# Performance work log

Measured on AMD Instinct MI355X. Metric: run time of the kernel, lower is better.

The kernel has to match this reference:

```python
import jax, jax.numpy as jnp
import numpy as np

N_NODES = 100000
N_EDGES = 3200000
F_IN = 128
F_HID = 32
F_OUT = 40


def gcn_conv(x, edge_index, edge_weight, W, b):
    # GCNConv with normalize=False: linear transform, then edge-weighted
    # gather from source nodes and scatter-add into destination nodes.
    h = x @ W                                   # [N, F_out]
    src, dst = edge_index[0], edge_index[1]
    msgs = h[src] * edge_weight[:, None]        # [E, F_out] gather + scale
    agg = jax.ops.segment_sum(msgs, dst, num_segments=N_NODES)
    return agg + b


def setup_inputs() -> dict:
    key = jax.random.key(0)
    k1, k2, k3, k4, k5, k6, k7 = jax.random.split(key, 7)
    x = jax.random.normal(k1, (N_NODES, F_IN), dtype=jnp.float32)
    edge_index = jax.random.randint(k2, (2, N_EDGES), 0, N_NODES, dtype=jnp.int64)
    edge_weight = jax.random.uniform(k3, (N_EDGES,), dtype=jnp.float32)
    # Glorot-style init for layer weights, zeros for biases (PyG defaults)
    W1 = jax.random.normal(k4, (F_IN, F_HID), dtype=jnp.float32) * (1.0 / np.sqrt(F_IN))
    b1 = jnp.zeros((F_HID,), dtype=jnp.float32)
    W2 = jax.random.normal(k5, (F_HID, F_OUT), dtype=jnp.float32) * (1.0 / np.sqrt(F_HID))
    b2 = jnp.zeros((F_OUT,), dtype=jnp.float32)
    return {"x": x, "edge_index": edge_index, "edge_weight": edge_weight,
            "W1": W1, "b1": b1, "W2": W2, "b2": b2}


def reference(x, edge_index, edge_weight, W1, b1, W2, b2):
    h = gcn_conv(x, edge_index, edge_weight, W1, b1)
    h = jax.nn.relu(h)
    # F.dropout(training=self.training) is identity in eval mode
    h = gcn_conv(h, edge_index, edge_weight, W2, b2)
    return jax.nn.log_softmax(h, axis=1)
```

## Files before the change

kernel.cpp:

```cpp
#include <hip/hip_runtime.h>
#include <hip/hip_fp16.h>
#include <math.h>

#define N_NODES 100000
#define N_EDGES 3200000
#define F_IN    128
#define F_HID   32
#define F_OUT   40
#define NBINS   ((N_NODES + 255) >> 8)
#define EPB     4096
#define NBLK    ((N_EDGES + EPB - 1) / EPB)
#define SRC_SPLIT 50000
#define CAPH    (N_EDGES / 2 + 8 * N_NODES)

typedef _Float16 h2_t __attribute__((ext_vector_type(2)));
__device__ __forceinline__ float fdot2u(unsigned a, unsigned b, float c) {
    return __builtin_amdgcn_fdot2(__builtin_bit_cast(h2_t, a),
                                  __builtin_bit_cast(h2_t, b), c, false);
}

__global__ __launch_bounds__(256) void gemm1_kernel(const float* __restrict__ x,
                                                    const float* __restrict__ W,
                                                    __half* __restrict__ h1h) {
    __shared__ float Ws[F_IN * F_HID];
    __shared__ float Xs[32][F_IN + 4];
    const int tid  = threadIdx.x;
    const int row0 = blockIdx.x * 32;

    for (int i = tid; i < (F_IN * F_HID) / 4; i += 256)
        ((float4*)Ws)[i] = ((const float4*)W)[i];

    for (int i = tid; i < 1024; i += 256) {
        int r = i >> 5;
        int c = i & 31;
        ((float4*)&Xs[r][0])[c] = ((const float4*)x)[(size_t)(row0 + r) * (F_IN / 4) + c];
    }
    __syncthreads();

    const int r  = tid >> 3;
    const int c0 = (tid & 7) * 4;
    float a0 = 0.f, a1 = 0.f, a2 = 0.f, a3 = 0.f;
    for (int k = 0; k < F_IN; ++k) {
        const float xv = Xs[r][k];
        const float* wrow = &Ws[k * F_HID + c0];
        a0 += xv * wrow[0];
        a1 += xv * wrow[1];
        a2 += xv * wrow[2];
        a3 += xv * wrow[3];
    }
    const int row = row0 + r;
    __half2* o = (__half2*)(h1h + (size_t)row * F_HID + c0);
    o[0] = __floats2half2_rn(a0, a1);
    o[1] = __floats2half2_rn(a2, a3);
}

__global__ __launch_bounds__(256) void histA_kernel(const int* __restrict__ ei,
                                                    int* __restrict__ gcnt) {
    __shared__ int lh[NBINS];
    const int tid = threadIdx.x;
    const int e0  = blockIdx.x * EPB;
    for (int i = tid; i < NBINS; i += 256) lh[i] = 0;
    __syncthreads();

    for (int base = 0; base < EPB; base += 1024) {
        const int e = e0 + base + 4 * tid;
        if (e + 3 < N_EDGES) {
            const int4 dv = *(const int4*)&ei[N_EDGES + e];
            atomicAdd(&lh[dv.x >> 8], 1);
            atomicAdd(&lh[dv.y >> 8], 1);
            atomicAdd(&lh[dv.z >> 8], 1);
            atomicAdd(&lh[dv.w >> 8], 1);
        } else {
            for (int k = 0; k < 4; ++k)
                if (e + k < N_EDGES) atomicAdd(&lh[ei[N_EDGES + e + k] >> 8], 1);
        }
    }
    __syncthreads();
    for (int b = tid; b < NBINS; b += 256)
        gcnt[(size_t)blockIdx.x * NBINS + b] = lh[b];
}

__global__ __launch_bounds__(256) void colscan_kernel(const int* __restrict__ gcnt,
                                                      int* __restrict__ pbase,
                                                      int* __restrict__ bintot) {
    __shared__ int s[256];
    __shared__ int carry;
    const int b   = blockIdx.x;
    const int tid = threadIdx.x;
    if (tid == 0) carry = 0;
    __syncthreads();
    for (int c = 0; c < NBLK; c += 256) {
        const int blk = c + tid;
        const int v = (blk < NBLK) ? gcnt[(size_t)blk * NBINS + b] : 0;
        s[tid] = v;
        __syncthreads();
        for (int off = 1; off < 256; off <<= 1) {
            int u = (tid >= off) ? s[tid - off] : 0;
            __syncthreads();
            s[tid] += u;
            __syncthreads();
        }
        if (blk < NBLK) pbase[(size_t)blk * NBINS + b] = carry + s[tid] - v;
        __syncthreads();
        if (tid == 255) carry += s[255];
        __syncthreads();
    }
    if (tid == 0) bintot[b] = carry;
}

__global__ __launch_bounds__(512) void binscan_kernel(const int* __restrict__ bintot,
                                                      int* __restrict__ binbase) {
    __shared__ int s[512];
    const int t = threadIdx.x;
    const int v = (t < NBINS) ? bintot[t] : 0;
    s[t] = v;
    __syncthreads();
    for (int off = 1; off < 512; off <<= 1) {
        int u = (t >= off) ? s[t - off] : 0;
        __syncthreads();
        s[t] += u;
        __syncthreads();
    }
    if (t <= NBINS) binbase[t] = s[t] - v;
}

__global__ __launch_bounds__(256) void placeA_kernel(const int* __restrict__ ei,
                                                     const float* __restrict__ ew,
                                                     const int* __restrict__ gcnt,
                                                     const int* __restrict__ binbase,
                                                     const int* __restrict__ pbase,
                                                     int* __restrict__ stg4,
                                                     unsigned short* __restrict__ metag) {
    __shared__ int lhist[512];
    __shared__ int lscan[512];
    __shared__ int lcur[512];
    __shared__ int lwbase[512];
    __shared__ int stmp[256];
    __shared__ int lstg4[EPB];
    __shared__ unsigned short lbin[EPB];
    __shared__ unsigned short lmeta[EPB];
    const int tid = threadIdx.x;
    const int blk = blockIdx.x;
    const int e0  = blk * EPB;
    const int tot = min(EPB, N_EDGES - e0);

    lhist[tid] = 0; lhist[tid + 256] = 0;
    lwbase[tid] = 0; lwbase[tid + 256] = 0;
    __syncthreads();
    for (int b = tid; b < NBINS; b += 256) {
        lhist[b]  = gcnt[(size_t)blk * NBINS + b];
        lwbase[b] = binbase[b] + pbase[(size_t)blk * NBINS + b];
    }
    __syncthreads();

    const int ca = lhist[2 * tid];
    const int cb = lhist[2 * tid + 1];
    const int pair = ca + cb;
    stmp[tid] = pair;
    __syncthreads();
    for (int off = 1; off < 256; off <<= 1) {
        int u = (tid >= off) ? stmp[tid - off] : 0;
        __syncthreads();
        stmp[tid] += u;
        __syncthreads();
    }
    const int pexcl = stmp[tid] - pair;
    lscan[2 * tid]     = pexcl;
    lscan[2 * tid + 1] = pexcl + ca;
    lcur[2 * tid]      = pexcl;
    lcur[2 * tid + 1]  = pexcl + ca;
    __syncthreads();

#define PLACE1(S, D, WF)                                                        \
    {                                                                           \
        const int b = (D) >> 8;                                                 \
        const int p = atomicAdd(&lcur[b], 1);                                   \
        lstg4[p] = (S) | ((int)__half_as_ushort(__float2half(WF)) << 17);       \
        lbin[p] = (unsigned short)b;                                            \
        lmeta[p] = (unsigned short)(((D) & 255) | (((S) >= SRC_SPLIT) << 8));   \
    }
    for (int base = 0; base < EPB; base += 1024) {
        const int e = e0 + base + 4 * tid;
        if (e + 3 < N_EDGES) {
            const int4   sv = *(const int4*)&ei[e];
            const int4   dv = *(const int4*)&ei[N_EDGES + e];
            const float4 wv = *(const float4*)&ew[e];
            PLACE1(sv.x, dv.x, wv.x);
            PLACE1(sv.y, dv.y, wv.y);
            PLACE1(sv.z, dv.z, wv.z);
            PLACE1(sv.w, dv.w, wv.w);
        } else {
            for (int k = 0; k < 4; ++k)
                if (e + k < N_EDGES)
                    PLACE1(ei[e + k], ei[N_EDGES + e + k], ew[e + k]);
        }
    }
#undef PLACE1
    __syncthreads();

    for (int i = tid; i < tot; i += 256) {
        const int b = lbin[i];
        const int pos = lwbase[b] + (i - lscan[b]);
        stg4[pos] = lstg4[i];
        metag[pos] = lmeta[i];
    }
}

__global__ __launch_bounds__(256) void partB1_kernel(const int* __restrict__ binbase,
                                                     const unsigned short* __restrict__ metag,
                                                     int* __restrict__ offsIBA,
                                                     int* __restrict__ offsIBB,
                                                     int* __restrict__ pbtA,
                                                     int* __restrict__ pbtB) {
    __shared__ int lcA[256], lcB[256], lsc[256];
    const int tid   = threadIdx.x;
    const int b     = blockIdx.x;
    const int start = binbase[b];
    const int end   = binbase[b + 1];

    lcA[tid] = 0; lcB[tid] = 0;
    __syncthreads();
    for (int j = start + tid; j < end; j += 256) {
        const unsigned m = metag[j];
        if (m & 256) atomicAdd(&lcB[m & 255], 1);
        else         atomicAdd(&lcA[m & 255], 1);
    }
    __syncthreads();

    const int padA = (lcA[tid] + 7) & ~7;
    lsc[tid] = padA;
    __syncthreads();
    for (int off = 1; off < 256; off <<= 1) {
        int u = (tid >= off) ? lsc[tid - off] : 0;
        __syncthreads();
        lsc[tid] += u;
        __syncthreads();
    }
    offsIBA[(b << 8) + tid] = lsc[tid] - padA;
    if (tid == 255) pbtA[b] = lsc[255];
    __syncthreads();

    const int padB = (lcB[tid] + 7) & ~7;
    lsc[tid] = padB;
    __syncthreads();
    for (int off = 1; off < 256; off <<= 1) {
        int u = (tid >= off) ? lsc[tid - off] : 0;
        __syncthreads();
        lsc[tid] += u;
        __syncthreads();
    }
    offsIBB[(b << 8) + tid] = lsc[tid] - padB;
    if (tid == 255) pbtB[b] = lsc[255];
}

__global__ __launch_bounds__(512) void padscan2_kernel(const int* __restrict__ pbtA,
                                                       const int* __restrict__ pbtB,
                                                       int* __restrict__ pbbA,
                                                       int* __restrict__ pbbB,
                                                       int* __restrict__ offsA,
                                                       int* __restrict__ offsB) {
    __shared__ int s[512];
    const int t = threadIdx.x;
    {
        const int v = (t < NBINS) ? pbtA[t] : 0;
        s[t] = v;
        __syncthreads();
        for (int off = 1; off < 512; off <<= 1) {
            int u = (t >= off) ? s[t - off] : 0;
            __syncthreads();
            s[t] += u;
            __syncthreads();
        }
        if (t <= NBINS) pbbA[t] = s[t] - v;
        if (t == NBINS) offsA[N_NODES] = s[t] - v;
        __syncthreads();
    }
    {
        const int v = (t < NBINS) ? pbtB[t] : 0;
        s[t] = v;
        __syncthreads();
        for (int off = 1; off < 512; off <<= 1) {
            int u = (t >= off) ? s[t - off] : 0;
            __syncthreads();
            s[t] += u;
            __syncthreads();
        }
        if (t <= NBINS) pbbB[t] = s[t] - v;
        if (t == NBINS) offsB[N_NODES] = s[t] - v;
    }
}

__global__ __launch_bounds__(256) void partB2_kernel(const int* __restrict__ binbase,
                                                     const int* __restrict__ stg4,
                                                     const unsigned short* __restrict__ metag,
                                                     const int* __restrict__ pbbA,
                                                     const int* __restrict__ pbbB,
                                                     const int* __restrict__ offsIBA,
                                                     const int* __restrict__ offsIBB,
                                                     int* __restrict__ offsA,
                                                     int* __restrict__ offsB,
                                                     int* __restrict__ bktA,
                                                     int* __restrict__ bktB) {
    __shared__ int lcurA[256], lcurB[256];
    const int tid  = threadIdx.x;
    const int b    = blockIdx.x;
    const int node = (b << 8) + tid;
    const int baseA = pbbA[b] + offsIBA[node];
    const int baseB = pbbB[b] + offsIBB[node];
    const int pendA = (tid < 255) ? (pbbA[b] + offsIBA[node + 1]) : pbbA[b + 1];
    const int pendB = (tid < 255) ? (pbbB[b] + offsIBB[node + 1]) : pbbB[b + 1];
    lcurA[tid] = baseA;
    lcurB[tid] = baseB;
    if (node < N_NODES) { offsA[node] = baseA; offsB[node] = baseB; }
    __syncthreads();

    const int start = binbase[b];
    const int end   = binbase[b + 1];
    for (int j = start + tid; j < end; j += 256) {
        const int word = stg4[j];
        const unsigned m = metag[j];
        if (m & 256) {
            const int pos = atomicAdd(&lcurB[m & 255], 1);
            bktB[pos] = word;
        } else {
            const int pos = atomicAdd(&lcurA[m & 255], 1);
            bktA[pos] = word;
        }
    }
    __syncthreads();

    for (int k = lcurA[tid]; k < pendA; ++k) bktA[k] = 0;
    for (int k = lcurB[tid]; k < pendB; ++k) bktB[k] = SRC_SPLIT;
}

__device__ __forceinline__ void gather_grp(const int* __restrict__ bkt,
                                           int j, const int jend,
                                           const char* __restrict__ tbl,
                                           const unsigned sub8,
                                           float& a0, float& a1, float& a2, float& a3) {
#define PAIR_BODY(PX, PY, RA, RB)                                               \
    {                                                                           \
        const unsigned wp = __builtin_amdgcn_perm((unsigned)(PY) >> 17,         \
                                                  (unsigned)(PX) >> 17,         \
                                                  0x05040100u);                 \
        a0 = fdot2u(__builtin_amdgcn_perm((RB).x, (RA).x, 0x05040100u), wp, a0);\
        a1 = fdot2u(__builtin_amdgcn_perm((RB).x, (RA).x, 0x07060302u), wp, a1);\
        a2 = fdot2u(__builtin_amdgcn_perm((RB).y, (RA).y, 0x05040100u), wp, a2);\
        a3 = fdot2u(__builtin_amdgcn_perm((RB).y, (RA).y, 0x07060302u), wp, a3);\
    }
#define TBL(P) (*(const uint2*)(tbl + (((unsigned)(P) & 0x1FFFFu) << 6) + sub8))
    for (; j < jend; j += 8) {
        const int4 p0 = *(const int4*)&bkt[j];
        const int4 p1 = *(const int4*)&bkt[j + 4];
        const uint2 r0 = TBL(p0.x);
        const uint2 r1 = TBL(p0.y);
        const uint2 r2 = TBL(p0.z);
        const uint2 r3 = TBL(p0.w);
        const uint2 r4 = TBL(p1.x);
        const uint2 r5 = TBL(p1.y);
        const uint2 r6 = TBL(p1.z);
        const uint2 r7 = TBL(p1.w);
        PAIR_BODY(p0.x, p0.y, r0, r1);
        PAIR_BODY(p0.z, p0.w, r2, r3);
        PAIR_BODY(p1.x, p1.y, r4, r5);
        PAIR_BODY(p1.z, p1.w, r6, r7);
    }
#undef TBL
#undef PAIR_BODY
}

__global__ __launch_bounds__(256) void gather1_kernel(const int* __restrict__ offsA,
                                                      const int* __restrict__ offsB,
                                                      const int* __restrict__ bktA,
                                                      const int* __restrict__ bktB,
                                                      const __half* __restrict__ h1h,
                                                      const float* __restrict__ b1,
                                                      __half* __restrict__ rh) {
    const int tid  = threadIdx.x;
    const int node = blockIdx.x * 32 + (tid >> 3);
    const int sub  = tid & 7;
    const unsigned sub8 = sub * 8;

    float a0 = 0.f, a1 = 0.f, a2 = 0.f, a3 = 0.f;
    gather_grp(bktA, offsA[node], offsA[node + 1], (const char*)h1h, sub8,
               a0, a1, a2, a3);
    gather_grp(bktB, offsB[node], offsB[node + 1], (const char*)h1h, sub8,
               a0, a1, a2, a3);

    const float4 bb = ((const float4*)b1)[sub];
    a0 = fmaxf(a0 + bb.x, 0.f);
    a1 = fmaxf(a1 + bb.y, 0.f);
    a2 = fmaxf(a2 + bb.z, 0.f);
    a3 = fmaxf(a3 + bb.w, 0.f);
    uint2 o;
    *(__half2*)&o.x = __floats2half2_rn(a0, a1);
    *(__half2*)&o.y = __floats2half2_rn(a2, a3);
    *(uint2*)((char*)rh + (size_t)node * 64 + sub8) = o;
}

__global__ __launch_bounds__(256) void gather2_lsm_kernel(const int* __restrict__ offsA,
                                                          const int* __restrict__ offsB,
                                                          const int* __restrict__ bktA,
                                                          const int* __restrict__ bktB,
                                                          const __half* __restrict__ rh,
                                                          const float* __restrict__ W2,
                                                          const float* __restrict__ b2,
                                                          float* __restrict__ out) {
    __shared__ float W2s[F_HID * F_OUT];
    __shared__ float sblk[32][F_HID + 1];
    const int tid = threadIdx.x;
    for (int i = tid; i < F_HID * F_OUT; i += 256) W2s[i] = W2[i];
    __syncthreads();

    const int nn   = tid >> 3;
    const int node = blockIdx.x * 32 + nn;
    const int sub  = tid & 7;
    const unsigned sub8 = sub * 8;

    float a0 = 0.f, a1 = 0.f, a2 = 0.f, a3 = 0.f;
    gather_grp(bktA, offsA[node], offsA[node + 1], (const char*)rh, sub8,
               a0, a1, a2, a3);
    gather_grp(bktB, offsB[node], offsB[node + 1], (const char*)rh, sub8,
               a0, a1, a2, a3);

    sblk[nn][sub * 4 + 0] = a0;
    sblk[nn][sub * 4 + 1] = a1;
    sblk[nn][sub * 4 + 2] = a2;
    sblk[nn][sub * 4 + 3] = a3;

    float o0 = b2[sub], o1 = b2[sub + 8], o2 = b2[sub + 16],
          o3 = b2[sub + 24], o4 = b2[sub + 32];
    #pragma unroll
    for (int k = 0; k < F_HID; ++k) {
        const float sv = sblk[nn][k];
        const float* wr = &W2s[k * F_OUT + sub];
        o0 += sv * wr[0];
        o1 += sv * wr[8];
        o2 += sv * wr[16];
        o3 += sv * wr[24];
        o4 += sv * wr[32];
    }

    float m = fmaxf(fmaxf(fmaxf(o0, o1), fmaxf(o2, o3)), o4);
    m = fmaxf(m, __shfl_xor(m, 1));
    m = fmaxf(m, __shfl_xor(m, 2));
    m = fmaxf(m, __shfl_xor(m, 4));
    float ex = __expf(o0 - m) + __expf(o1 - m) + __expf(o2 - m)
             + __expf(o3 - m) + __expf(o4 - m);
    ex += __shfl_xor(ex, 1);
    ex += __shfl_xor(ex, 2);
    ex += __shfl_xor(ex, 4);
    const float ls = m + __logf(ex);

    float* op = out + (size_t)node * F_OUT + sub;
    op[0]  = o0 - ls;
    op[8]  = o1 - ls;
    op[16] = o2 - ls;
    op[24] = o3 - ls;
    op[32] = o4 - ls;
}

extern "C" void kernel_launch(void* const* d_in, const int* in_sizes, int n_in,
                              void* d_out, int out_size, void* d_ws, size_t ws_size,
                              hipStream_t stream) {
    const float* x  = (const float*)d_in[0];
    const int*   ei = (const int*)d_in[1];
    const float* ew = (const float*)d_in[2];
    const float* W1 = (const float*)d_in[3];
    const float* b1 = (const float*)d_in[4];
    const float* W2 = (const float*)d_in[5];
    const float* b2 = (const float*)d_in[6];
    float* out = (float*)d_out;

    char* p = (char*)d_ws;
    size_t off = 0;
    auto alloc = [&](size_t bytes) {
        char* r = p + off;
        off += (bytes + 15) & ~(size_t)15;
        return r;
    };
    int*   gcnt    = (int*)  alloc((size_t)NBLK * NBINS * 4);
    int*   pbase   = (int*)  alloc((size_t)NBLK * NBINS * 4);
    int*   bintot  = (int*)  alloc((size_t)NBINS * 4);
    int*   binbase = (int*)  alloc((size_t)(NBINS + 1) * 4);
    int*   pbtA    = (int*)  alloc((size_t)NBINS * 4);
    int*   pbtB    = (int*)  alloc((size_t)NBINS * 4);
    int*   pbbA    = (int*)  alloc((size_t)(NBINS + 1) * 4);
    int*   pbbB    = (int*)  alloc((size_t)(NBINS + 1) * 4);
    int*   offsIBA = (int*)  alloc((size_t)NBINS * 256 * 4);
    int*   offsIBB = (int*)  alloc((size_t)NBINS * 256 * 4);
    int*   offsA   = (int*)  alloc((size_t)(N_NODES + 1) * 4);
    int*   offsB   = (int*)  alloc((size_t)(N_NODES + 1) * 4);
    int*   bktA    = (int*)  alloc((size_t)CAPH * 4);
    int*   bktB    = (int*)  alloc((size_t)CAPH * 4);
    char*  uni     = (char*) alloc((size_t)N_EDGES * 6);
    int*   stg4    = (int*)uni;
    unsigned short* metag = (unsigned short*)(uni + (size_t)N_EDGES * 4);
    __half* h1h    = (__half*)uni;
    __half* rh     = h1h + (size_t)N_NODES * F_HID;

    histA_kernel<<<NBLK, 256, 0, stream>>>(ei, gcnt);
    colscan_kernel<<<NBINS, 256, 0, stream>>>(gcnt, pbase, bintot);
    binscan_kernel<<<1, 512, 0, stream>>>(bintot, binbase);
    placeA_kernel<<<NBLK, 256, 0, stream>>>(ei, ew, gcnt, binbase, pbase, stg4, metag);
    partB1_kernel<<<NBINS, 256, 0, stream>>>(binbase, metag, offsIBA, offsIBB, pbtA, pbtB);
    padscan2_kernel<<<1, 512, 0, stream>>>(pbtA, pbtB, pbbA, pbbB, offsA, offsB);
    partB2_kernel<<<NBINS, 256, 0, stream>>>(binbase, stg4, metag, pbbA, pbbB,
                                             offsIBA, offsIBB, offsA, offsB, bktA, bktB);

    gemm1_kernel<<<N_NODES / 32, 256, 0, stream>>>(x, W1, h1h);
    gather1_kernel<<<N_NODES / 32, 256, 0, stream>>>(offsA, offsB, bktA, bktB, h1h, b1, rh);

    gather2_lsm_kernel<<<N_NODES / 32, 256, 0, stream>>>(offsA, offsB, bktA, bktB, rh, W2, b2, out);
}
```

Before: 177.5 us.

## Sort nodes by padded degree class to balance gather work per block

Adds a counting sort of nodes by padded in-degree (histogram, scan, placement kernels) that produces a permutation. The two gather kernels then process nodes in permuted order, so nodes with similar edge counts share a wavefront and lanes diverge less in loop trip count. In exchange it launches three extra small kernels plus a memset, and the output writes per block become scattered rather than contiguous. With random uniform edges the degree spread is narrow, so there is little imbalance to remove.

```diff
diff --git a/kernel.cpp b/kernel.cpp
--- a/kernel.cpp
+++ b/kernel.cpp
@@ -12,6 +12,7 @@
 #define NBLK    ((N_EDGES + EPB - 1) / EPB)
 #define SRC_SPLIT 50000
 #define CAPH    (N_EDGES / 2 + 8 * N_NODES)
+#define NCLS    64
 
 typedef _Float16 h2_t __attribute__((ext_vector_type(2)));
 __device__ __forceinline__ float fdot2u(unsigned a, unsigned b, float c) {
@@ -333,6 +334,66 @@
     for (int k = lcurB[tid]; k < pendB; ++k) bktB[k] = SRC_SPLIT;
 }
 
+__global__ __launch_bounds__(256) void deghist_kernel(const int* __restrict__ offsA,
+                                                      const int* __restrict__ offsB,
+                                                      int* __restrict__ dcnt) {
+    __shared__ int lc[NCLS];
+    const int tid = threadIdx.x;
+    if (tid < NCLS) lc[tid] = 0;
+    __syncthreads();
+    const int n = blockIdx.x * 256 + tid;
+    if (n < N_NODES) {
+        const int len = (offsA[n + 1] - offsA[n]) + (offsB[n + 1] - offsB[n]);
+        atomicAdd(&lc[min(len >> 3, NCLS - 1)], 1);
+    }
+    __syncthreads();
+    if (tid < NCLS && lc[tid]) atomicAdd(&dcnt[tid], lc[tid]);
+}
+
+__global__ __launch_bounds__(64) void degscan_kernel(const int* __restrict__ dcnt,
+                                                     int* __restrict__ dcur) {
+    __shared__ int s[NCLS];
+    const int t = threadIdx.x;
+    const int v = dcnt[t];
+    s[t] = v;
+    __syncthreads();
+    for (int off = 1; off < NCLS; off <<= 1) {
+        int u = (t >= off) ? s[t - off] : 0;
+        __syncthreads();
+        s[t] += u;
+        __syncthreads();
+    }
+    dcur[t] = s[t] - v;
+}
+
+__global__ __launch_bounds__(256) void degplace_kernel(const int* __restrict__ offsA,
+                                                       const int* __restrict__ offsB,
+                                                       int* __restrict__ dcur,
+                                                       int* __restrict__ perm) {
+    __shared__ int lcnt[NCLS], lbase[NCLS];
+    const int tid = threadIdx.x;
+    if (tid < NCLS) lcnt[tid] = 0;
+    __syncthreads();
+    const int n = blockIdx.x * 256 + tid;
+    int cls = 0;
+    if (n < N_NODES) {
+        const int len = (offsA[n + 1] - offsA[n]) + (offsB[n + 1] - offsB[n]);
+        cls = min(len >> 3, NCLS - 1);
+        atomicAdd(&lcnt[cls], 1);
+    }
+    __syncthreads();
+    if (tid < NCLS) {
+        const int c = lcnt[tid];
+        lbase[tid] = c ? atomicAdd(&dcur[tid], c) : 0;
+        lcnt[tid] = 0;
+    }
+    __syncthreads();
+    if (n < N_NODES) {
+        const int r = atomicAdd(&lcnt[cls], 1);
+        perm[lbase[cls] + r] = n;
+    }
+}
+
 __device__ __forceinline__ void gather_grp(const int* __restrict__ bkt,
                                            int j, const int jend,
                                            const char* __restrict__ tbl,
@@ -369,7 +430,8 @@
 #undef PAIR_BODY
 }
 
-__global__ __launch_bounds__(256) void gather1_kernel(const int* __restrict__ offsA,
+__global__ __launch_bounds__(256) void gather1_kernel(const int* __restrict__ perm,
+                                                      const int* __restrict__ offsA,
                                                       const int* __restrict__ offsB,
                                                       const int* __restrict__ bktA,
                                                       const int* __restrict__ bktB,
@@ -377,7 +439,7 @@
                                                       const float* __restrict__ b1,
                                                       __half* __restrict__ rh) {
     const int tid  = threadIdx.x;
-    const int node = blockIdx.x * 32 + (tid >> 3);
+    const int node = perm[blockIdx.x * 32 + (tid >> 3)];
     const int sub  = tid & 7;
     const unsigned sub8 = sub * 8;
 
@@ -398,7 +460,8 @@
     *(uint2*)((char*)rh + (size_t)node * 64 + sub8) = o;
 }
 
-__global__ __launch_bounds__(256) void gather2_lsm_kernel(const int* __restrict__ offsA,
+__global__ __launch_bounds__(256) void gather2_lsm_kernel(const int* __restrict__ perm,
+                                                          const int* __restrict__ offsA,
                                                           const int* __restrict__ offsB,
                                                           const int* __restrict__ bktA,
                                                           const int* __restrict__ bktB,
@@ -413,7 +476,7 @@
     __syncthreads();
 
     const int nn   = tid >> 3;
-    const int node = blockIdx.x * 32 + nn;
+    const int node = perm[blockIdx.x * 32 + nn];
     const int sub  = tid & 7;
     const unsigned sub8 = sub * 8;
 
@@ -487,10 +550,13 @@
     int*   pbtB    = (int*)  alloc((size_t)NBINS * 4);
     int*   pbbA    = (int*)  alloc((size_t)(NBINS + 1) * 4);
     int*   pbbB    = (int*)  alloc((size_t)(NBINS + 1) * 4);
+    int*   dcnt    = (int*)  alloc((size_t)NCLS * 4);
+    int*   dcur    = (int*)  alloc((size_t)NCLS * 4);
     int*   offsIBA = (int*)  alloc((size_t)NBINS * 256 * 4);
     int*   offsIBB = (int*)  alloc((size_t)NBINS * 256 * 4);
     int*   offsA   = (int*)  alloc((size_t)(N_NODES + 1) * 4);
     int*   offsB   = (int*)  alloc((size_t)(N_NODES + 1) * 4);
+    int*   perm    = (int*)  alloc((size_t)N_NODES * 4);
     int*   bktA    = (int*)  alloc((size_t)CAPH * 4);
     int*   bktB    = (int*)  alloc((size_t)CAPH * 4);
     char*  uni     = (char*) alloc((size_t)N_EDGES * 6);
@@ -498,6 +564,8 @@
     unsigned short* metag = (unsigned short*)(uni + (size_t)N_EDGES * 4);
     __half* h1h    = (__half*)uni;
     __half* rh     = h1h + (size_t)N_NODES * F_HID;
+
+    const int nnodeblk = (N_NODES + 255) / 256;
 
     histA_kernel<<<NBLK, 256, 0, stream>>>(ei, gcnt);
     colscan_kernel<<<NBINS, 256, 0, stream>>>(gcnt, pbase, bintot);
@@ -508,8 +576,13 @@
     partB2_kernel<<<NBINS, 256, 0, stream>>>(binbase, stg4, metag, pbbA, pbbB,
                                              offsIBA, offsIBB, offsA, offsB, bktA, bktB);
 
+    hipMemsetAsync(dcnt, 0, NCLS * 4, stream);
+    deghist_kernel<<<nnodeblk, 256, 0, stream>>>(offsA, offsB, dcnt);
+    degscan_kernel<<<1, 64, 0, stream>>>(dcnt, dcur);
+    degplace_kernel<<<nnodeblk, 256, 0, stream>>>(offsA, offsB, dcur, perm);
+
     gemm1_kernel<<<N_NODES / 32, 256, 0, stream>>>(x, W1, h1h);
-    gather1_kernel<<<N_NODES / 32, 256, 0, stream>>>(offsA, offsB, bktA, bktB, h1h, b1, rh);
-
-    gather2_lsm_kernel<<<N_NODES / 32, 256, 0, stream>>>(offsA, offsB, bktA, bktB, rh, W2, b2, out);
-}
+    gather1_kernel<<<N_NODES / 32, 256, 0, stream>>>(perm, offsA, offsB, bktA, bktB, h1h, b1, rh);
+
+    gather2_lsm_kernel<<<N_NODES / 32, 256, 0, stream>>>(perm, offsA, offsB, bktA, bktB, rh, W2, b2, out);
+}
```

New measurement: 198.8 us. 12.0% more time.
